# Performance work log

Measured on AMD Instinct MI355X. Metric: run time of the kernel, lower is better.

## Reference

```python
import math
import jax, jax.numpy as jnp
import numpy as np

K = 1.0            # Lorentz manifold curvature k
B, S = 4, 2048     # batch, seq_len
IN, H, OUT = 512, 8, 64   # in_channels, num_heads, out_channels (space dim; head_dim = OUT+1)


def setup_inputs() -> dict:
    key = jax.random.key(0)
    ks = jax.random.split(key, 8)
    std = 1.0 / math.sqrt(IN)
    return {
        "query_input": jax.random.normal(ks[0], (B, S, IN), jnp.float32),
        "source_input": jax.random.normal(ks[1], (B, S, IN), jnp.float32),
        # per-head HypLinear weights stacked on a leading head axis: [H, OUT, IN]
        "Wq_w": jax.random.normal(ks[2], (H, OUT, IN), jnp.float32) * std,
        "Wq_b": jnp.zeros((H, OUT), jnp.float32),
        "Wk_w": jax.random.normal(ks[3], (H, OUT, IN), jnp.float32) * std,
        "Wk_b": jnp.zeros((H, OUT), jnp.float32),
        "Wv_w": jax.random.normal(ks[4], (H, OUT, IN), jnp.float32) * std,
        "Wv_b": jnp.zeros((H, OUT), jnp.float32),
        "scale": jnp.array([math.sqrt(OUT)], jnp.float32),  # nn.Parameter([sqrt(out_channels)])
        "bias": jnp.zeros((), jnp.float32),                 # nn.Parameter(zeros(()))
    }


def hyp_linear(x, w, b):
    # HypLinear: linear map to space part, recompute Lorentz time coord sqrt(||x_s||^2 + k)
    sp = jnp.einsum('bsi,hoi->bsho', x, w) + b            # [B,S,H,OUT]
    t = jnp.sqrt(jnp.sum(sp * sp, axis=-1, keepdims=True) + K)
    return jnp.concatenate([t, sp], axis=-1)              # [B,S,H,OUT+1]


def reference(query_input, source_input, Wq_w, Wq_b, Wk_w, Wk_b, Wv_w, Wv_b, scale, bias):
    q = hyp_linear(query_input, Wq_w, Wq_b)   # [B,S,H,D], D = OUT+1
    k = hyp_linear(source_input, Wk_w, Wk_b)
    v = hyp_linear(source_input, Wv_w, Wv_b)

    # Lorentzian cinner: <x,y>_L = -x0*y0 + <x_s, y_s>
    sgn = jnp.concatenate([-jnp.ones((1,), q.dtype), jnp.ones((OUT,), q.dtype)])
    att = jnp.einsum('bqhd,bkhd->bhqk', q * sgn, k)       # [B,H,S,S]
    att = (2.0 + 2.0 * att) / scale[0] + bias

    causal = jnp.triu(jnp.full((S, S), -1e9, q.dtype), 1)  # causal mask (additive)
    att = jax.nn.softmax(att + causal, axis=-1)

    ctx = jnp.einsum('bhqk,bkhd->bqhd', att, v)           # [B,S,H,D]

    # manifold.mid_point over the heads axis (dim=-2)
    ave = jnp.mean(ctx, axis=2)                           # [B,S,D]
    inner = -ave[..., :1] ** 2 + jnp.sum(ave[..., 1:] ** 2, axis=-1, keepdims=True)
    denom = jnp.sqrt(jnp.maximum(jnp.abs(-inner), 1e-8))
    return math.sqrt(K) * ave / denom                     # [B,S,D]
```

## Files before the change

### kernel.cpp

```cpp
#include <hip/hip_runtime.h>

#define BATCH 4
#define SEQ   2048
#define INC   512
#define NH    8
#define OUTC  64
#define DD    65

typedef float f32x4 __attribute__((ext_vector_type(4)));
typedef short short8 __attribute__((ext_vector_type(8)));
typedef short short4v __attribute__((ext_vector_type(4)));
typedef unsigned int uint2v __attribute__((ext_vector_type(2)));
typedef unsigned short us;

static __device__ __forceinline__ us f2b(float f) {
  unsigned int u = __float_as_uint(f);
  u = (u + 0x7FFFu + ((u >> 16) & 1u)) >> 16;
  return (us)u;
}
static __device__ __forceinline__ float b2f(us h) {
  return __uint_as_float(((unsigned int)h) << 16);
}
static __device__ __forceinline__ unsigned int pk2(float lo, float hi) {
  unsigned int r;
  asm("v_cvt_pk_bf16_f32 %0, %1, %2" : "=v"(r) : "v"(lo), "v"(hi));
  return r;
}

#define GLDS(g, l) __builtin_amdgcn_global_load_lds( \
    (const __attribute__((address_space(1))) void*)(g), \
    (__attribute__((address_space(3))) void*)(l), 16, 0, 0)

__global__ __launch_bounds__(256) void tobf16_kernel(
    const float* __restrict__ Xq, const float* __restrict__ Xs,
    const float* __restrict__ Wq, const float* __restrict__ Wk,
    const float* __restrict__ Wv,
    us* __restrict__ dXq, us* __restrict__ dXs,
    us* __restrict__ dWq, us* __restrict__ dWk, us* __restrict__ dWv)
{
  const int which = blockIdx.y;
  const float* src;
  us* dst;
  int n;
  switch (which) {
    case 0: src = Xq; dst = dXq; n = BATCH * SEQ * INC; break;
    case 1: src = Xs; dst = dXs; n = BATCH * SEQ * INC; break;
    case 2: src = Wq; dst = dWq; n = NH * OUTC * INC; break;
    case 3: src = Wk; dst = dWk; n = NH * OUTC * INC; break;
    default: src = Wv; dst = dWv; n = NH * OUTC * INC; break;
  }
  for (long i = (long)blockIdx.x * 256 + threadIdx.x; i * 4 < n;
       i += (long)gridDim.x * 256) {
    f32x4 v = *(const f32x4*)(src + i * 4);
    short4v o;
    o[0] = (short)f2b(v[0]); o[1] = (short)f2b(v[1]);
    o[2] = (short)f2b(v[2]); o[3] = (short)f2b(v[3]);
    *(short4v*)(dst + i * 4) = o;
  }
}

__global__ __launch_bounds__(256) void proj_kernel(
    const us* __restrict__ Xqb, const us* __restrict__ Xsb,
    const us* __restrict__ Wqb, const us* __restrict__ Wkb, const us* __restrict__ Wvb,
    const float* __restrict__ Bq, const float* __restrict__ Bk, const float* __restrict__ Bv,
    us* __restrict__ qs, float* __restrict__ qt,
    us* __restrict__ ks, us* __restrict__ kta,
    us* __restrict__ vs, us* __restrict__ vth, us* __restrict__ vtl)
{
  const int which = blockIdx.z;
  const us* X = (which == 0) ? Xqb : Xsb;
  const us* W = (which == 0) ? Wqb : (which == 1 ? Wkb : Wvb);
  const float* Bb = (which == 0) ? Bq : (which == 1 ? Bk : Bv);
  us* outs = (which == 0) ? qs : (which == 1 ? ks : vs);

  const int m0 = blockIdx.x * 64;
  const int h  = blockIdx.y;
  const int n0 = h * 64;

  __shared__ alignas(16) us lX[2][64 * 64];
  __shared__ alignas(16) us lW[2][64 * 64];

  const int tid  = threadIdx.x;
  const int lane = tid & 63;
  const int wave = tid >> 6;
  const int arow = lane & 15;
  const int agrp = lane >> 4;
  const int rl   = lane >> 3;
  const int chx  = ((lane & 7) ^ rl) * 8;
  const int r0   = wave * 8 + rl;
  const int r1   = r0 + 32;

#define PSTAGE(buf, k0) do { \
    GLDS(X + (size_t)(m0 + r0) * INC + (k0) + chx, &lX[buf][wave * 512]); \
    GLDS(X + (size_t)(m0 + r1) * INC + (k0) + chx, &lX[buf][2048 + wave * 512]); \
    GLDS(W + (size_t)(n0 + r0) * INC + (k0) + chx, &lW[buf][wave * 512]); \
    GLDS(W + (size_t)(n0 + r1) * INC + (k0) + chx, &lW[buf][2048 + wave * 512]); \
  } while (0)

  f32x4 acc[4] = {};
  PSTAGE(0, 0);

  for (int kk = 0; kk < 8; ++kk) {
    const int cur = kk & 1;
    if (kk < 7) {
      PSTAGE(cur ^ 1, (kk + 1) * 64);
      asm volatile("s_waitcnt vmcnt(4)");
    } else {
      asm volatile("s_waitcnt vmcnt(0)");
    }
    __builtin_amdgcn_s_barrier();
#pragma unroll
    for (int kc = 0; kc < 2; ++kc) {
      short8 af = *(const short8*)&lX[cur][(wave * 16 + arow) * 64 + (((kc * 4 + agrp) ^ (arow & 7)) * 8)];
#pragma unroll
      for (int c = 0; c < 4; ++c) {
        short8 bf = *(const short8*)&lW[cur][(c * 16 + arow) * 64 + (((kc * 4 + agrp) ^ (arow & 7)) * 8)];
        acc[c] = __builtin_amdgcn_mfma_f32_16x16x32_bf16(af, bf, acc[c], 0, 0, 0);
      }
    }
    __builtin_amdgcn_s_barrier();
  }

  float bcol[4];
#pragma unroll
  for (int c = 0; c < 4; ++c) bcol[c] = Bb[n0 + c * 16 + arow];
#pragma unroll
  for (int r = 0; r < 4; ++r) {
    float s2 = 0.f;
#pragma unroll
    for (int c = 0; c < 4; ++c) {
      float v = acc[c][r] + bcol[c];
      acc[c][r] = v;
      s2 += v * v;
    }
    s2 += __shfl_xor(s2, 1); s2 += __shfl_xor(s2, 2);
    s2 += __shfl_xor(s2, 4); s2 += __shfl_xor(s2, 8);
    float tv = sqrtf(s2 + 1.0f);
    int gs = m0 + wave * 16 + agrp * 4 + r;
    int bi = gs >> 11, si = gs & (SEQ - 1);
    size_t rowbase = (size_t)(bi * NH + h) * SEQ + si;
    size_t obase = rowbase * 64;
#pragma unroll
    for (int c = 0; c < 4; ++c) outs[obase + c * 16 + arow] = f2b(acc[c][r]);
    if (arow == 0) {
      if (which == 0) {
        qt[rowbase] = tv;
      } else {
        us th = f2b(tv);
        us tl = f2b(tv - b2f(th));
        if (which == 1) {
          short8 row = {};
          row[0] = (short)(th ^ 0x8000);
          row[1] = (short)(tl ^ 0x8000);
          row[2] = (short)(th ^ 0x8000);
          *(short8*)&kta[rowbase * 8] = row;
        } else {
          vth[rowbase] = th;
          vtl[rowbase] = tl;
        }
      }
    }
  }
}

__global__ __launch_bounds__(256) void transpose_v_kernel(
    const us* __restrict__ vs, us* __restrict__ vT)
{
  const int bh = blockIdx.y;
  const int s0 = blockIdx.x * 64;
  __shared__ us lT[64 * 80];
  const int tid = threadIdx.x;
#pragma unroll
  for (int u0 = 0; u0 < 2; ++u0) {
    int u = tid + u0 * 256;
    int row = u >> 3, ch = u & 7;
    short8 v = *(const short8*)&vs[((size_t)bh * SEQ + s0 + row) * 64 + ch * 8];
    *(short8*)&lT[row * 80 + ch * 8] = v;
  }
  __syncthreads();
#pragma unroll
  for (int u0 = 0; u0 < 2; ++u0) {
    int u = tid + u0 * 256;
    int o = u >> 3, sc = u & 7;
    short8 w;
#pragma unroll
    for (int j = 0; j < 8; ++j) w[j] = lT[(sc * 8 + j) * 80 + o];
    *(short8*)&vT[((size_t)bh * 64 + o) * SEQ + s0 + sc * 8] = w;
  }
}

__global__ __launch_bounds__(256) void attn_kernel(
    const us* __restrict__ qs, const float* __restrict__ qt,
    const us* __restrict__ ks, const us* __restrict__ kta,
    const us* __restrict__ vT, const us* __restrict__ vth, const us* __restrict__ vtl,
    const float* __restrict__ scale_p, float* __restrict__ ctx)
{
  const int f = blockIdx.x + 16 * blockIdx.y;
  const int xcd = f & 7, slot = f >> 3;
  const int bh = xcd * 4 + (slot >> 4);
  const int xb = slot & 15;
  const float al2 = (2.0f / scale_p[0]) * 1.44269504088896f;

  __shared__ alignas(16) us lK[2][64 * 64];
  __shared__ alignas(16) us lV[2][64 * 64];
  __shared__ alignas(16) us lKt[2][64 * 8];
  __shared__ alignas(16) us lVt[2][512];
  __shared__ alignas(16) us lP[4][16 * 64];

  const int tid  = threadIdx.x;
  const int lane = tid & 63;
  const int wave = tid >> 6;
  const int arow = lane & 15;
  const int agrp = lane >> 4;

  const size_t bhbase = (size_t)bh * SEQ;
  const us* kgp  = ks  + bhbase * 64;
  const us* vgp  = vT  + (size_t)bh * 64 * SEQ;
  const us* ktg  = kta + bhbase * 8;
  const us* vthg = vth + bhbase;
  const us* vtlg = vtl + bhbase;

  const int rl   = lane >> 3;
  const int chx  = ((lane & 7) ^ rl) * 8;
  const int r0s  = wave * 8 + rl;
  const int r1s  = r0s + 32;
  const int dsl0 = (agrp ^ (arow & 7)) * 8;
  const int dsl1 = ((4 + agrp) ^ (arow & 7)) * 8;
  const int swE  = (arow & 7) * 8;
  us* myP = &lP[wave][0];

  const us* vtsrc = (((lane >> 3) & 1) ? vtlg : vthg) + (lane & 7) * 8;

#define ASTAGE(buf, k0) do { \
    GLDS(kgp + (size_t)((k0) + r0s) * 64 + chx, &lK[buf][wave * 512]); \
    GLDS(kgp + (size_t)((k0) + r1s) * 64 + chx, &lK[buf][2048 + wave * 512]); \
    GLDS(vgp + (size_t)r0s * SEQ + (k0) + chx, &lV[buf][wave * 512]); \
    GLDS(vgp + (size_t)r1s * SEQ + (k0) + chx, &lV[buf][2048 + wave * 512]); \
    GLDS(ktg + (size_t)((k0) + lane) * 8, &lKt[buf][0]); \
    GLDS(vtsrc + (k0), &lVt[buf][0]); \
  } while (0)

  short8 ones8;
#pragma unroll
  for (int j = 0; j < 8; ++j) ones8[j] = (short)0x3F80;

  for (int pp = 0; pp < 2; ++pp) {
    const int qb = pp ? (31 - xb) : xb;
    const int q0 = qb * 64;
    const int wq = wave * 16 + arow;

    ASTAGE(0, 0);

    const us* qp = qs + (bhbase + q0 + wq) * 64;
    short8 qf0 = *(const short8*)(qp + agrp * 8);
    short8 qf1 = *(const short8*)(qp + 32 + agrp * 8);
    float qtv = qt[bhbase + q0 + wq];
    us qh = f2b(qtv);
    us ql = f2b(qtv - b2f(qh));
    short8 qf2 = {};
    if (agrp == 0) { qf2[0] = (short)qh; qf2[1] = (short)qh; qf2[2] = (short)ql; }

    float m_ = -1e30f;
    f32x4 acc[5] = {};

    for (int kti = 0; kti <= qb; ++kti) {
      const int cur = kti & 1;
      if (kti < qb) {
        ASTAGE(cur ^ 1, (kti + 1) * 64);
        asm volatile("s_waitcnt vmcnt(6)");
      } else {
        asm volatile("s_waitcnt vmcnt(0)");
      }
      __builtin_amdgcn_s_barrier();

      const us* Kb  = lK[cur];
      const us* Vb  = lV[cur];
      const us* Ktb = lKt[cur];
      const us* Vtb = lVt[cur];

      f32x4 sS[4] = {};
      __builtin_amdgcn_s_setprio(1);
#pragma unroll
      for (int c = 0; c < 4; ++c) {
        short8 kf = *(const short8*)&Kb[(c * 16 + arow) * 64 + dsl0];
        sS[c] = __builtin_amdgcn_mfma_f32_16x16x32_bf16(kf, qf0, sS[c], 0, 0, 0);
      }
#pragma unroll
      for (int c = 0; c < 4; ++c) {
        short8 kf = *(const short8*)&Kb[(c * 16 + arow) * 64 + dsl1];
        sS[c] = __builtin_amdgcn_mfma_f32_16x16x32_bf16(kf, qf1, sS[c], 0, 0, 0);
      }
#pragma unroll
      for (int c = 0; c < 4; ++c) {
        short8 kf2 = {};
        if (agrp == 0) kf2 = *(const short8*)&Ktb[(c * 16 + arow) * 8];
        sS[c] = __builtin_amdgcn_mfma_f32_16x16x32_bf16(kf2, qf2, sS[c], 0, 0, 0);
      }
      __builtin_amdgcn_s_setprio(0);

      if (kti == qb) {
#pragma unroll
        for (int c = 0; c < 4; ++c)
#pragma unroll
          for (int r = 0; r < 4; ++r)
            if (c * 16 + agrp * 4 + r > wq) sS[c][r] = -1e30f;
      }

      float mx0 = fmaxf(fmaxf(sS[0][0], sS[0][1]), fmaxf(sS[0][2], sS[0][3]));
      float mx1 = fmaxf(fmaxf(sS[1][0], sS[1][1]), fmaxf(sS[1][2], sS[1][3]));
      float mx2 = fmaxf(fmaxf(sS[2][0], sS[2][1]), fmaxf(sS[2][2], sS[2][3]));
      float mx3 = fmaxf(fmaxf(sS[3][0], sS[3][1]), fmaxf(sS[3][2], sS[3][3]));
      float mx = fmaxf(fmaxf(mx0, mx1), fmaxf(mx2, mx3));
      mx = fmaxf(mx, __shfl_xor(mx, 16));
      mx = fmaxf(mx, __shfl_xor(mx, 32));
      float mn = fmaxf(m_, mx);
      float fac = exp2f(al2 * (m_ - mn));
      m_ = mn;
      float almn = al2 * mn;

#pragma unroll
      for (int c = 0; c < 4; ++c)
#pragma unroll
        for (int r = 0; r < 4; ++r)
          sS[c][r] = exp2f(fmaf(al2, sS[c][r], -almn));

#pragma unroll
      for (int r = 0; r < 4; ++r) {
        float facr = __shfl(fac, agrp * 4 + r);
        acc[0][r] *= facr; acc[1][r] *= facr; acc[2][r] *= facr;
        acc[3][r] *= facr; acc[4][r] *= facr;
      }

#pragma unroll
      for (int c = 0; c < 4; ++c) {
        uint2v w;
        w[0] = pk2(sS[c][0], sS[c][1]);
        w[1] = pk2(sS[c][2], sS[c][3]);
        *(uint2v*)&myP[arow * 64 + ((c * 16 + agrp * 4) ^ swE)] = w;
      }

      __builtin_amdgcn_s_setprio(1);
#pragma unroll
      for (int kc = 0; kc < 2; ++kc) {
        short8 pf = *(const short8*)&myP[arow * 64 + ((kc * 32 + agrp * 8) ^ swE)];
        const int dsl = kc ? dsl1 : dsl0;
#pragma unroll
        for (int dc = 0; dc < 4; ++dc) {
          short8 vf = *(const short8*)&Vb[(dc * 16 + arow) * 64 + dsl];
          acc[dc] = __builtin_amdgcn_mfma_f32_16x16x32_bf16(pf, vf, acc[dc], 0, 0, 0);
        }
        short8 vf4 = {};
        if (arow < 2)  vf4 = *(const short8*)&Vtb[arow * 64 + kc * 32 + agrp * 8];
        if (arow == 2) vf4 = ones8;
        acc[4] = __builtin_amdgcn_mfma_f32_16x16x32_bf16(pf, vf4, acc[4], 0, 0, 0);
      }
      __builtin_amdgcn_s_setprio(0);

      __builtin_amdgcn_s_barrier();
    }

#pragma unroll
    for (int r = 0; r < 4; ++r) {
      float ls = __shfl(acc[4][r], (agrp << 4) | 2);
      float t0 = __shfl(acc[4][r], (agrp << 4) | 0);
      float t1 = __shfl(acc[4][r], (agrp << 4) | 1);
      float invr = 1.0f / ls;
      size_t rb = (bhbase + q0 + wave * 16 + agrp * 4 + r) * (size_t)DD;
      if (arow == 0) ctx[rb] = (t0 + t1) * invr;
#pragma unroll
      for (int dc = 0; dc < 4; ++dc)
        ctx[rb + 1 + dc * 16 + arow] = acc[dc][r] * invr;
    }
  }
}

__global__ __launch_bounds__(256) void finalize_kernel(
    const float* __restrict__ ctx, float* __restrict__ out)
{
  const int tid  = threadIdx.x;
  const int lane = tid & 63;
  const int gw = blockIdx.x * 4 + (tid >> 6);
  const int b = gw >> 11, si = gw & (SEQ - 1);
  float v = 0.f, v64 = 0.f;
#pragma unroll
  for (int h = 0; h < NH; ++h) {
    size_t base = ((size_t)(b * NH + h) * SEQ + si) * (size_t)DD;
    v += ctx[base + lane];
    if (lane == 0) v64 += ctx[base + 64];
  }
  float ave   = v * 0.125f;
  float ave64 = v64 * 0.125f;
  float contrib = (lane == 0) ? (ave64 * ave64 - ave * ave) : ave * ave;
  contrib += __shfl_xor(contrib, 1);
  contrib += __shfl_xor(contrib, 2);
  contrib += __shfl_xor(contrib, 4);
  contrib += __shfl_xor(contrib, 8);
  contrib += __shfl_xor(contrib, 16);
  contrib += __shfl_xor(contrib, 32);
  float denom = sqrtf(fmaxf(fabsf(contrib), 1e-8f));
  size_t ob = ((size_t)b * SEQ + si) * (size_t)DD;
  out[ob + lane] = ave / denom;
  if (lane == 0) out[ob + 64] = ave64 / denom;
}

extern "C" void kernel_launch(void* const* d_in, const int* in_sizes, int n_in,
                              void* d_out, int out_size, void* d_ws, size_t ws_size,
                              hipStream_t stream) {
  const float* Xq  = (const float*)d_in[0];
  const float* Xs  = (const float*)d_in[1];
  const float* Wq  = (const float*)d_in[2];
  const float* Bq  = (const float*)d_in[3];
  const float* Wk  = (const float*)d_in[4];
  const float* Bk  = (const float*)d_in[5];
  const float* Wv  = (const float*)d_in[6];
  const float* Bv  = (const float*)d_in[7];
  const float* scale = (const float*)d_in[8];
  float* out = (float*)d_out;

  char* p = (char*)d_ws;
  const size_t NROW = (size_t)BATCH * NH * SEQ;

  float* ctx = (float*)p;
  us* Xqb = (us*)p;
  us* Xsb = (us*)(p + 8388608);
  p += 17040128;
  us* Wqb16 = (us*)p; p += 524288;
  us* Wkb16 = (us*)p; p += 524288;
  us* Wvb16 = (us*)p; p += 524288;
  us* qsb = (us*)p; p += NROW * 64 * 2;
  us* ksb = (us*)p; p += NROW * 64 * 2;
  us* vsb = (us*)p; p += NROW * 64 * 2;
  us* vTb = (us*)p; p += NROW * 64 * 2;
  float* qtb = (float*)p; p += NROW * 4;
  us* ktaw = (us*)p; p += NROW * 8 * 2;
  us* vthw = (us*)p; p += NROW * 2;
  us* vtlw = (us*)p; p += NROW * 2;

  tobf16_kernel<<<dim3(1024, 5), 256, 0, stream>>>(
      Xq, Xs, Wq, Wk, Wv, Xqb, Xsb, Wqb16, Wkb16, Wvb16);
  proj_kernel<<<dim3(128, NH, 3), 256, 0, stream>>>(
      Xqb, Xsb, Wqb16, Wkb16, Wvb16, Bq, Bk, Bv,
      qsb, qtb, ksb, ktaw, vsb, vthw, vtlw);
  transpose_v_kernel<<<dim3(SEQ / 64, BATCH * NH), 256, 0, stream>>>(vsb, vTb);
  attn_kernel<<<dim3(16, BATCH * NH), 256, 0, stream>>>(
      qsb, qtb, ksb, ktaw, vTb, vthw, vtlw, scale, ctx);
  finalize_kernel<<<(BATCH * SEQ) / 4, 256, 0, stream>>>(ctx, out);
}
```

Measured before the change: 111.8 us.

## Split attention key range in halves with partial softmax merge in finalize

Each (head, query-block) pair is now handled by two blocks, each covering half of the causal key range with 32-key tiles. This doubles the grid and shrinks shared memory per block, aiming at better CU occupancy and load balance. The running max starts at zero and the accumulators are rescaled only when the max grows past a threshold, which cuts per-tile rescale work. Each block writes unnormalized partial sums plus its row max and row sum, and the finalize kernel merges the two halves before the head mid-point reduction. In exchange it adds extra partial-buffer traffic, issues more barriers per key, and uses smaller MFMA tiles.

```diff
diff --git a/kernel.cpp b/kernel.cpp
--- a/kernel.cpp
+++ b/kernel.cpp
@@ -30,6 +30,8 @@
 #define GLDS(g, l) __builtin_amdgcn_global_load_lds( \
     (const __attribute__((address_space(1))) void*)(g), \
     (__attribute__((address_space(3))) void*)(l), 16, 0, 0)
+
+#define MASKV (-60000.0f)
 
 __global__ __launch_bounds__(256) void tobf16_kernel(
     const float* __restrict__ Xq, const float* __restrict__ Xs,
@@ -193,19 +195,21 @@
     const us* __restrict__ qs, const float* __restrict__ qt,
     const us* __restrict__ ks, const us* __restrict__ kta,
     const us* __restrict__ vT, const us* __restrict__ vth, const us* __restrict__ vtl,
-    const float* __restrict__ scale_p, float* __restrict__ ctx)
+    const float* __restrict__ scale_p, float* __restrict__ part)
 {
-  const int f = blockIdx.x + 16 * blockIdx.y;
-  const int xcd = f & 7, slot = f >> 3;
-  const int bh = xcd * 4 + (slot >> 4);
-  const int xb = slot & 15;
+  const int f = blockIdx.x;
+  const int xcd = f & 7, idx = f >> 3;
+  const int bh = xcd * 4 + (idx >> 5);
+  const int inner = idx & 31;
+  const int xb = inner >> 1;
+  const int hf = inner & 1;
   const float al2 = (2.0f / scale_p[0]) * 1.44269504088896f;
 
-  __shared__ alignas(16) us lK[2][64 * 64];
-  __shared__ alignas(16) us lV[2][64 * 64];
-  __shared__ alignas(16) us lKt[2][64 * 8];
-  __shared__ alignas(16) us lVt[2][512];
-  __shared__ alignas(16) us lP[4][16 * 64];
+  __shared__ alignas(16) us lK[2][32 * 64];
+  __shared__ alignas(16) us lV[2][64 * 32];
+  __shared__ alignas(16) us lKt[2][32 * 8];
+  __shared__ alignas(16) us lVt[2][64];
+  __shared__ alignas(16) us lP[4][16 * 32];
 
   const int tid  = threadIdx.x;
   const int lane = tid & 63;
@@ -222,34 +226,39 @@
 
   const int rl   = lane >> 3;
   const int chx  = ((lane & 7) ^ rl) * 8;
-  const int r0s  = wave * 8 + rl;
-  const int r1s  = r0s + 32;
+  const int vdr  = lane >> 2;
+  const int vchx = ((lane & 3) ^ (vdr & 3)) * 8;
   const int dsl0 = (agrp ^ (arow & 7)) * 8;
   const int dsl1 = ((4 + agrp) ^ (arow & 7)) * 8;
-  const int swE  = (arow & 7) * 8;
+  const int psl  = (agrp ^ (arow & 3)) * 8;
   us* myP = &lP[wave][0];
 
-  const us* vtsrc = (((lane >> 3) & 1) ? vtlg : vthg) + (lane & 7) * 8;
-
-#define ASTAGE(buf, k0) do { \
-    GLDS(kgp + (size_t)((k0) + r0s) * 64 + chx, &lK[buf][wave * 512]); \
-    GLDS(kgp + (size_t)((k0) + r1s) * 64 + chx, &lK[buf][2048 + wave * 512]); \
-    GLDS(vgp + (size_t)r0s * SEQ + (k0) + chx, &lV[buf][wave * 512]); \
-    GLDS(vgp + (size_t)r1s * SEQ + (k0) + chx, &lV[buf][2048 + wave * 512]); \
-    GLDS(ktg + (size_t)((k0) + lane) * 8, &lKt[buf][0]); \
-    GLDS(vtsrc + (k0), &lVt[buf][0]); \
+#define ASTAGE(buf, t32) do { \
+    const int kk0 = (t32) * 32; \
+    _Pragma("unroll") \
+    for (int g = 0; g < 4; ++g) \
+      GLDS(kgp + (size_t)(kk0 + 8 * g + rl) * 64 + chx, &lK[buf][g * 512]); \
+    _Pragma("unroll") \
+    for (int g = 0; g < 4; ++g) \
+      GLDS(vgp + (size_t)(16 * g + vdr) * SEQ + kk0 + vchx, &lV[buf][g * 512]); \
+    if (lane < 32) GLDS(ktg + (size_t)(kk0 + lane) * 8, &lKt[buf][0]); \
+    if (lane < 4)  GLDS(vthg + kk0 + lane * 8, &lVt[buf][0]); \
+    if (lane < 4)  GLDS(vtlg + kk0 + lane * 8, &lVt[buf][32]); \
   } while (0)
 
   short8 ones8;
 #pragma unroll
   for (int j = 0; j < 8; ++j) ones8[j] = (short)0x3F80;
 
-  for (int pp = 0; pp < 2; ++pp) {
-    const int qb = pp ? (31 - xb) : xb;
+  for (int seg = 0; seg < 2; ++seg) {
+    const int qb = seg ? (31 - xb) : xb;
     const int q0 = qb * 64;
+    const int nt = qb + 1;
+    const int tstart = hf * nt;
     const int wq = wave * 16 + arow;
-
-    ASTAGE(0, 0);
+    const int qg = q0 + wq;
+
+    ASTAGE(0, tstart);
 
     const us* qp = qs + (bhbase + q0 + wq) * 64;
     short8 qf0 = *(const short8*)(qp + agrp * 8);
@@ -260,14 +269,15 @@
     short8 qf2 = {};
     if (agrp == 0) { qf2[0] = (short)qh; qf2[1] = (short)qh; qf2[2] = (short)ql; }
 
-    float m_ = -1e30f;
+    float m_ = 0.0f;
     f32x4 acc[5] = {};
 
-    for (int kti = 0; kti <= qb; ++kti) {
-      const int cur = kti & 1;
-      if (kti < qb) {
-        ASTAGE(cur ^ 1, (kti + 1) * 64);
-        asm volatile("s_waitcnt vmcnt(6)");
+    for (int it = 0; it < nt; ++it) {
+      const int t = tstart + it;
+      const int cur = it & 1;
+      if (it < nt - 1) {
+        ASTAGE(cur ^ 1, t + 1);
+        asm volatile("s_waitcnt vmcnt(11)");
       } else {
         asm volatile("s_waitcnt vmcnt(0)");
       }
@@ -278,119 +288,135 @@
       const us* Ktb = lKt[cur];
       const us* Vtb = lVt[cur];
 
-      f32x4 sS[4] = {};
+      f32x4 sS[2] = {};
       __builtin_amdgcn_s_setprio(1);
 #pragma unroll
-      for (int c = 0; c < 4; ++c) {
+      for (int c = 0; c < 2; ++c) {
         short8 kf = *(const short8*)&Kb[(c * 16 + arow) * 64 + dsl0];
         sS[c] = __builtin_amdgcn_mfma_f32_16x16x32_bf16(kf, qf0, sS[c], 0, 0, 0);
       }
 #pragma unroll
-      for (int c = 0; c < 4; ++c) {
+      for (int c = 0; c < 2; ++c) {
         short8 kf = *(const short8*)&Kb[(c * 16 + arow) * 64 + dsl1];
         sS[c] = __builtin_amdgcn_mfma_f32_16x16x32_bf16(kf, qf1, sS[c], 0, 0, 0);
       }
 #pragma unroll
-      for (int c = 0; c < 4; ++c) {
+      for (int c = 0; c < 2; ++c) {
         short8 kf2 = {};
         if (agrp == 0) kf2 = *(const short8*)&Ktb[(c * 16 + arow) * 8];
         sS[c] = __builtin_amdgcn_mfma_f32_16x16x32_bf16(kf2, qf2, sS[c], 0, 0, 0);
       }
       __builtin_amdgcn_s_setprio(0);
 
-      if (kti == qb) {
-#pragma unroll
-        for (int c = 0; c < 4; ++c)
+      if (t >= 2 * qb) {
+        const int kb = t * 32;
+#pragma unroll
+        for (int c = 0; c < 2; ++c)
 #pragma unroll
           for (int r = 0; r < 4; ++r)
-            if (c * 16 + agrp * 4 + r > wq) sS[c][r] = -1e30f;
-      }
-
-      float mx0 = fmaxf(fmaxf(sS[0][0], sS[0][1]), fmaxf(sS[0][2], sS[0][3]));
-      float mx1 = fmaxf(fmaxf(sS[1][0], sS[1][1]), fmaxf(sS[1][2], sS[1][3]));
-      float mx2 = fmaxf(fmaxf(sS[2][0], sS[2][1]), fmaxf(sS[2][2], sS[2][3]));
-      float mx3 = fmaxf(fmaxf(sS[3][0], sS[3][1]), fmaxf(sS[3][2], sS[3][3]));
-      float mx = fmaxf(fmaxf(mx0, mx1), fmaxf(mx2, mx3));
+            if (kb + c * 16 + agrp * 4 + r > qg) sS[c][r] = MASKV;
+      }
+
+      float mx = fmaxf(fmaxf(fmaxf(sS[0][0], sS[0][1]), fmaxf(sS[0][2], sS[0][3])),
+                       fmaxf(fmaxf(sS[1][0], sS[1][1]), fmaxf(sS[1][2], sS[1][3])));
       mx = fmaxf(mx, __shfl_xor(mx, 16));
       mx = fmaxf(mx, __shfl_xor(mx, 32));
-      float mn = fmaxf(m_, mx);
-      float fac = exp2f(al2 * (m_ - mn));
-      m_ = mn;
-      float almn = al2 * mn;
-
-#pragma unroll
-      for (int c = 0; c < 4; ++c)
+      if (__any(mx > m_ + 20.0f)) {
+        float mn = fmaxf(m_, mx);
+        float fac = exp2f(al2 * (m_ - mn));
+        m_ = mn;
+#pragma unroll
+        for (int r = 0; r < 4; ++r) {
+          float facr = __shfl(fac, agrp * 4 + r);
+          acc[0][r] *= facr; acc[1][r] *= facr; acc[2][r] *= facr;
+          acc[3][r] *= facr; acc[4][r] *= facr;
+        }
+      }
+      const float alm = al2 * m_;
+#pragma unroll
+      for (int c = 0; c < 2; ++c)
 #pragma unroll
         for (int r = 0; r < 4; ++r)
-          sS[c][r] = exp2f(fmaf(al2, sS[c][r], -almn));
-
-#pragma unroll
-      for (int r = 0; r < 4; ++r) {
-        float facr = __shfl(fac, agrp * 4 + r);
-        acc[0][r] *= facr; acc[1][r] *= facr; acc[2][r] *= facr;
-        acc[3][r] *= facr; acc[4][r] *= facr;
-      }
-
-#pragma unroll
-      for (int c = 0; c < 4; ++c) {
+          sS[c][r] = exp2f(fmaf(al2, sS[c][r], -alm));
+
+#pragma unroll
+      for (int c = 0; c < 2; ++c) {
         uint2v w;
         w[0] = pk2(sS[c][0], sS[c][1]);
         w[1] = pk2(sS[c][2], sS[c][3]);
-        *(uint2v*)&myP[arow * 64 + ((c * 16 + agrp * 4) ^ swE)] = w;
+        int g = c * 2 + (agrp >> 1);
+        int eW = ((g ^ (arow & 3)) * 8) + (agrp & 1) * 4;
+        *(uint2v*)&myP[arow * 32 + eW] = w;
       }
 
       __builtin_amdgcn_s_setprio(1);
-#pragma unroll
-      for (int kc = 0; kc < 2; ++kc) {
-        short8 pf = *(const short8*)&myP[arow * 64 + ((kc * 32 + agrp * 8) ^ swE)];
-        const int dsl = kc ? dsl1 : dsl0;
-#pragma unroll
-        for (int dc = 0; dc < 4; ++dc) {
-          short8 vf = *(const short8*)&Vb[(dc * 16 + arow) * 64 + dsl];
-          acc[dc] = __builtin_amdgcn_mfma_f32_16x16x32_bf16(pf, vf, acc[dc], 0, 0, 0);
-        }
-        short8 vf4 = {};
-        if (arow < 2)  vf4 = *(const short8*)&Vtb[arow * 64 + kc * 32 + agrp * 8];
-        if (arow == 2) vf4 = ones8;
-        acc[4] = __builtin_amdgcn_mfma_f32_16x16x32_bf16(pf, vf4, acc[4], 0, 0, 0);
-      }
+      short8 pf = *(const short8*)&myP[arow * 32 + psl];
+#pragma unroll
+      for (int dc = 0; dc < 4; ++dc) {
+        short8 vf = *(const short8*)&Vb[(dc * 16 + arow) * 32 + psl];
+        acc[dc] = __builtin_amdgcn_mfma_f32_16x16x32_bf16(pf, vf, acc[dc], 0, 0, 0);
+      }
+      short8 vf4 = {};
+      if (arow < 2)  vf4 = *(const short8*)&Vtb[arow * 32 + agrp * 8];
+      if (arow == 2) vf4 = ones8;
+      acc[4] = __builtin_amdgcn_mfma_f32_16x16x32_bf16(pf, vf4, acc[4], 0, 0, 0);
       __builtin_amdgcn_s_setprio(0);
 
       __builtin_amdgcn_s_barrier();
     }
 
+    const size_t pb = ((size_t)(bh * 32 + qb) * 2 + hf) * 64;
 #pragma unroll
     for (int r = 0; r < 4; ++r) {
-      float ls = __shfl(acc[4][r], (agrp << 4) | 2);
       float t0 = __shfl(acc[4][r], (agrp << 4) | 0);
       float t1 = __shfl(acc[4][r], (agrp << 4) | 1);
-      float invr = 1.0f / ls;
-      size_t rb = (bhbase + q0 + wave * 16 + agrp * 4 + r) * (size_t)DD;
-      if (arow == 0) ctx[rb] = (t0 + t1) * invr;
+      float ls = __shfl(acc[4][r], (agrp << 4) | 2);
+      float mr = __shfl(m_, agrp * 4 + r);
+      size_t rp = (pb + wave * 16 + agrp * 4 + r) * 68;
 #pragma unroll
       for (int dc = 0; dc < 4; ++dc)
-        ctx[rb + 1 + dc * 16 + arow] = acc[dc][r] * invr;
+        part[rp + dc * 16 + arow] = acc[dc][r];
+      if (arow == 0) {
+        part[rp + 64] = t0 + t1;
+        part[rp + 65] = ls;
+        part[rp + 66] = mr;
+      }
     }
   }
 }
 
 __global__ __launch_bounds__(256) void finalize_kernel(
-    const float* __restrict__ ctx, float* __restrict__ out)
+    const float* __restrict__ part, const float* __restrict__ scale_p,
+    float* __restrict__ out)
 {
   const int tid  = threadIdx.x;
   const int lane = tid & 63;
   const int gw = blockIdx.x * 4 + (tid >> 6);
   const int b = gw >> 11, si = gw & (SEQ - 1);
-  float v = 0.f, v64 = 0.f;
+  const int qb = si >> 6, row = si & 63;
+  const float al2 = (2.0f / scale_p[0]) * 1.44269504088896f;
+
+  float vsum = 0.f, tsum = 0.f;
 #pragma unroll
   for (int h = 0; h < NH; ++h) {
-    size_t base = ((size_t)(b * NH + h) * SEQ + si) * (size_t)DD;
-    v += ctx[base + lane];
-    if (lane == 0) v64 += ctx[base + 64];
-  }
-  float ave   = v * 0.125f;
-  float ave64 = v64 * 0.125f;
-  float contrib = (lane == 0) ? (ave64 * ave64 - ave * ave) : ave * ave;
+    const size_t tile = (size_t)(b * NH + h) * 32 + qb;
+    const size_t b0 = (tile * 2 * 64 + row) * 68;
+    const size_t b1 = ((tile * 2 + 1) * 64 + row) * 68;
+    float A1 = part[b0 + lane];
+    float A2 = part[b1 + lane];
+    float T1 = part[b0 + 64], L1 = part[b0 + 65], M1 = part[b0 + 66];
+    float T2 = part[b1 + 64], L2 = part[b1 + 65], M2 = part[b1 + 66];
+    float ms = fmaxf(M1, M2);
+    float f1 = exp2f(al2 * (M1 - ms));
+    float f2 = exp2f(al2 * (M2 - ms));
+    float inv = 1.0f / (f1 * L1 + f2 * L2);
+    vsum = fmaf(fmaf(f1, A1, f2 * A2), inv, vsum);
+    tsum = fmaf(fmaf(f1, T1, f2 * T2), inv, tsum);
+  }
+  float ave  = vsum * 0.125f;
+  float tave = tsum * 0.125f;
+  float contrib = ave * ave;
+  if (lane == 0) contrib -= tave * tave;
   contrib += __shfl_xor(contrib, 1);
   contrib += __shfl_xor(contrib, 2);
   contrib += __shfl_xor(contrib, 4);
@@ -399,8 +425,8 @@
   contrib += __shfl_xor(contrib, 32);
   float denom = sqrtf(fmaxf(fabsf(contrib), 1e-8f));
   size_t ob = ((size_t)b * SEQ + si) * (size_t)DD;
-  out[ob + lane] = ave / denom;
-  if (lane == 0) out[ob + 64] = ave64 / denom;
+  out[ob + 1 + lane] = ave / denom;
+  if (lane == 0) out[ob] = tave / denom;
 }
 
 extern "C" void kernel_launch(void* const* d_in, const int* in_sizes, int n_in,
@@ -420,13 +446,13 @@
   char* p = (char*)d_ws;
   const size_t NROW = (size_t)BATCH * NH * SEQ;
 
-  float* ctx = (float*)p;
-  us* Xqb = (us*)p;
-  us* Xsb = (us*)(p + 8388608);
-  p += 17040128;
-  us* Wqb16 = (us*)p; p += 524288;
-  us* Wkb16 = (us*)p; p += 524288;
-  us* Wvb16 = (us*)p; p += 524288;
+  float* part = (float*)p;
+  us* Xqb   = (us*)p;
+  us* Xsb   = (us*)(p + 16777216);
+  us* Wqb16 = (us*)(p + 33554432);
+  us* Wkb16 = (us*)(p + 34078720);
+  us* Wvb16 = (us*)(p + 34603008);
+  p += (size_t)1024 * 2 * 64 * 68 * 4;
   us* qsb = (us*)p; p += NROW * 64 * 2;
   us* ksb = (us*)p; p += NROW * 64 * 2;
   us* vsb = (us*)p; p += NROW * 64 * 2;
@@ -442,7 +468,7 @@
       Xqb, Xsb, Wqb16, Wkb16, Wvb16, Bq, Bk, Bv,
       qsb, qtb, ksb, ktaw, vsb, vthw, vtlw);
   transpose_v_kernel<<<dim3(SEQ / 64, BATCH * NH), 256, 0, stream>>>(vsb, vTb);
-  attn_kernel<<<dim3(16, BATCH * NH), 256, 0, stream>>>(
-      qsb, qtb, ksb, ktaw, vTb, vthw, vtlw, scale, ctx);
-  finalize_kernel<<<(BATCH * SEQ) / 4, 256, 0, stream>>>(ctx, out);
-}
+  attn_kernel<<<dim3(1024), 256, 0, stream>>>(
+      qsb, qtb, ksb, ktaw, vTb, vthw, vtlw, scale, part);
+  finalize_kernel<<<(BATCH * SEQ) / 4, 256, 0, stream>>>(part, scale, out);
+}
```

Measured after the change: 167.4 us. 1.5x slower.
